# Kernel optimization log

Measured on AMD Instinct MI355X. Metric: run time of the kernel, lower is better.

Reference implementation:

```python
import jax, jax.numpy as jnp
import numpy as np

N_NODES = 100000
N_EDGES = 3200000
NFEAT, NHID1, NHID2, NCLASS = 512, 16, 64, 16
NEG_SLOPE = 0.01  # torch F.leaky_relu default


def setup_inputs() -> dict:
    key = jax.random.key(0)
    ks = jax.random.split(key, 10)
    x = jax.random.normal(ks[0], (N_NODES, NFEAT), dtype=jnp.float32)
    src = jax.random.randint(ks[1], (N_EDGES,), 0, N_NODES, dtype=jnp.int32)
    dst = jax.random.randint(ks[2], (N_EDGES,), 0, N_NODES, dtype=jnp.int32)
    edge_vals = jax.random.uniform(ks[3], (N_EDGES,), dtype=jnp.float32)
    def glorot(k, fan_in, fan_out):
        s = 1.0 / np.sqrt(fan_in)
        return jax.random.uniform(k, (fan_in, fan_out), dtype=jnp.float32, minval=-s, maxval=s)
    W1 = glorot(ks[4], NFEAT, NHID1)
    b1 = jnp.zeros((NHID1,), dtype=jnp.float32)
    W2 = glorot(ks[5], NHID1, NHID2)
    b2 = jnp.zeros((NHID2,), dtype=jnp.float32)
    W3 = glorot(ks[6], NHID2, NCLASS)
    b3 = jnp.zeros((NCLASS,), dtype=jnp.float32)
    return dict(x=x, src=src, dst=dst, edge_vals=edge_vals,
                W1=W1, b1=b1, W2=W2, b2=b2, W3=W3, b3=b3)


def _gcn_layer(h, src, dst, edge_vals, W, b):
    # support = h @ W  [N, F_out]; out = spmm(adj, support) + b
    support = h @ W
    msgs = edge_vals[:, None] * support[src]            # gather + scale per edge
    agg = jax.ops.segment_sum(msgs, dst, num_segments=N_NODES)  # scatter-add
    return agg + b


def reference(x, src, dst, edge_vals, W1, b1, W2, b2, W3, b3):
    h1 = jax.nn.leaky_relu(_gcn_layer(x, src, dst, edge_vals, W1, b1), NEG_SLOPE)
    h2 = jax.nn.leaky_relu(_gcn_layer(h1, src, dst, edge_vals, W2, b2), NEG_SLOPE)
    h3 = _gcn_layer(h2, src, dst, edge_vals, W3, b3)
    return jax.nn.log_softmax(h3, axis=1)
```

## Files before the change

### kernel.cpp

```cpp
#include <hip/hip_runtime.h>
#include <cmath>


#define BD 64
#define NBKT 1563
#define NBLK 2048
#define SORT_CAP 3072

typedef __attribute__((ext_vector_type(8))) short bf16x8;
typedef __attribute__((ext_vector_type(4))) float f32x4;

__device__ __forceinline__ short to_bf16(float f) {
    unsigned u = __float_as_uint(f);
    u += 0x8000u;
    return (short)(u >> 16);
}
__device__ __forceinline__ unsigned pack2bf(float a, float b) {
    return (unsigned)(unsigned short)to_bf16(a) |
           ((unsigned)(unsigned short)to_bf16(b) << 16);
}
__device__ __forceinline__ float bf_lo(unsigned v) {
    return __uint_as_float(v << 16);
}
__device__ __forceinline__ float bf_hi(unsigned v) {
    return __uint_as_float(v & 0xFFFF0000u);
}

__global__ __launch_bounds__(256) void p1g_k(const float* __restrict__ x,
                                             const float* __restrict__ W1,
                                             unsigned short* __restrict__ t1,
                                             const int* __restrict__ dst,
                                             int* __restrict__ C,
                                             int N, int E, int NB_gemm) {
    __shared__ __align__(16) unsigned short wlds[8192];
    if ((int)blockIdx.x < NB_gemm) {
        {
            int t = threadIdx.x;
            int kt = t >> 4, col = t & 15;
#pragma unroll
            for (int j = 0; j < 32; ++j) {
                int k = kt * 32 + j;
                float v = W1[(size_t)k * 16 + col];
                wlds[(((kt * 4 + (j >> 3)) * 16 + col) << 3) + (j & 7)] =
                    (unsigned short)to_bf16(v);
            }
        }
        __syncthreads();
        int wid = (blockIdx.x * 256 + (int)threadIdx.x) >> 6;
        int ntiles = (N + 15) >> 4;
        if (wid >= ntiles) return;
        int lane = threadIdx.x & 63;
        int m = lane & 15, kg = lane >> 4;
        int r = wid * 16 + m;
        int rc = r < N ? r : N - 1;
        const float4* Xv = reinterpret_cast<const float4*>(x + (size_t)rc * 512);
        f32x4 acc = {0.f, 0.f, 0.f, 0.f};
#pragma unroll
        for (int kt = 0; kt < 16; ++kt) {
            float4 xa = Xv[kt * 8 + kg * 2];
            float4 xb = Xv[kt * 8 + kg * 2 + 1];
            bf16x8 a;
            a[0] = to_bf16(xa.x); a[1] = to_bf16(xa.y);
            a[2] = to_bf16(xa.z); a[3] = to_bf16(xa.w);
            a[4] = to_bf16(xb.x); a[5] = to_bf16(xb.y);
            a[6] = to_bf16(xb.z); a[7] = to_bf16(xb.w);
            bf16x8 b = *reinterpret_cast<const bf16x8*>(
                &wlds[((kt * 4 + kg) * 16 + m) << 3]);
            acc = __builtin_amdgcn_mfma_f32_16x16x32_bf16(a, b, acc, 0, 0, 0);
        }
#pragma unroll
        for (int i = 0; i < 4; ++i) {
            int ro = wid * 16 + kg * 4 + i;
            if (ro < N) t1[(size_t)ro * 16 + m] = (unsigned short)to_bf16(acc[i]);
        }
        return;
    }
    int* h = (int*)wlds;
    int k = (int)blockIdx.x - NB_gemm;
    for (int i = threadIdx.x; i < NBKT; i += 256) h[i] = 0;
    __syncthreads();
    int epb = (E + NBLK - 1) / NBLK;
    int lo = k * epb, hi = min(lo + epb, E);
    for (int e = lo + (int)threadIdx.x; e < hi; e += 256)
        atomicAdd(&h[dst[e] >> 6], 1);
    __syncthreads();
    for (int i = threadIdx.x; i < NBKT; i += 256)
        C[(size_t)k * NBKT + i] = h[i];
}

__global__ __launch_bounds__(256) void p2a(int* __restrict__ C,
                                           int* __restrict__ btot) {
    __shared__ int s[16][17];
    int bs = threadIdx.x & 15, ki = threadIdx.x >> 4;
    int b = blockIdx.x * 16 + bs;
    bool ok = b < NBKT;
    int sum = 0;
    if (ok) {
        for (int j = 0; j < 128; ++j)
            sum += C[(size_t)(ki * 128 + j) * NBKT + b];
    }
    s[ki][bs] = sum;
    __syncthreads();
    int base = 0;
    for (int j = 0; j < ki; ++j) base += s[j][bs];
    if (ok) {
        if (ki == 15) btot[b] = base + sum;
        int run = base;
        for (int j = 0; j < 128; ++j) {
            size_t idx = (size_t)(ki * 128 + j) * NBKT + b;
            int v = C[idx];
            C[idx] = run;
            run += v;
        }
    }
}

__global__ __launch_bounds__(256) void p2b(const int* __restrict__ btot,
                                           int* __restrict__ bbase, int E) {
    __shared__ int ps[256];
    int loc[8], sum = 0;
    int base = (int)threadIdx.x * 8;
#pragma unroll
    for (int j = 0; j < 8; ++j) {
        int i = base + j;
        int v = (i < NBKT) ? btot[i] : 0;
        loc[j] = sum; sum += v;
    }
    ps[threadIdx.x] = sum;
    __syncthreads();
    for (int st = 1; st < 256; st <<= 1) {
        int tv = (threadIdx.x >= (unsigned)st) ? ps[threadIdx.x - st] : 0;
        __syncthreads();
        ps[threadIdx.x] += tv;
        __syncthreads();
    }
    int prev = ps[threadIdx.x] - sum;
#pragma unroll
    for (int j = 0; j < 8; ++j) {
        int i = base + j;
        if (i <= NBKT) bbase[i] = prev + loc[j];
    }
}

__global__ __launch_bounds__(256) void p3_place(const int* __restrict__ src,
                                                const int* __restrict__ dst,
                                                const float* __restrict__ ev,
                                                const int* __restrict__ C,
                                                const int* __restrict__ bbase,
                                                int2* __restrict__ recA, int E) {
    __shared__ int cur[NBKT];
    int bid = (int)blockIdx.x;
    int k = ((bid & 7) << 8) | (bid >> 3);
    for (int i = threadIdx.x; i < NBKT; i += 256)
        cur[i] = bbase[i] + C[(size_t)k * NBKT + i];
    __syncthreads();
    int epb = (E + NBLK - 1) / NBLK;
    int lo = k * epb, hi = min(lo + epb, E);
    for (int e = lo + (int)threadIdx.x; e < hi; e += 256) {
        int d = dst[e];
        int p = atomicAdd(&cur[d >> 6], 1);
        recA[p] = make_int2(src[e] | ((d & 63) << 17), __float_as_int(ev[e]));
    }
}

__device__ __forceinline__ int pack_rec(int srcbits, float evf) {
    int q = (int)(evf * 32768.f + 0.5f);
    q = q > 32767 ? 32767 : q;
    return (srcbits << 15) | q;
}

__global__ __launch_bounds__(256) void sort2_k(const int* __restrict__ bbase,
                                               const int2* __restrict__ recA,
                                               int* __restrict__ recB,
                                               int* __restrict__ off,
                                               int N, int E) {
    __shared__ int2 ls[SORT_CAP];
    __shared__ int lo_[SORT_CAP];
    __shared__ int cnt[BD];
    __shared__ int cur[BD];
    int b = blockIdx.x;
    int e0 = bbase[b], e1 = bbase[b + 1], n = e1 - e0;
    if (threadIdx.x < BD) cnt[threadIdx.x] = 0;
    __syncthreads();
    if (n <= SORT_CAP) {
        for (int i = threadIdx.x; i < n; i += 256) {
            int2 r = recA[e0 + i];
            ls[i] = r;
            atomicAdd(&cnt[(r.x >> 17) & 63], 1);
        }
        __syncthreads();
        if (threadIdx.x < 64) {
            int v = cnt[threadIdx.x];
            int inc = v;
#pragma unroll
            for (int s = 1; s < 64; s <<= 1) {
                int t = __shfl_up(inc, s, 64);
                if ((int)threadIdx.x >= s) inc += t;
            }
            int excl = inc - v;
            cur[threadIdx.x] = excl;
            int node = b * BD + (int)threadIdx.x;
            if (node < N) off[node] = e0 + excl;
        }
        if (threadIdx.x == 64 && b == (int)gridDim.x - 1) off[N] = E;
        __syncthreads();
        for (int i = threadIdx.x; i < n; i += 256) {
            int2 r = ls[i];
            int p = atomicAdd(&cur[(r.x >> 17) & 63], 1);
            lo_[p] = pack_rec(r.x & 0x1FFFF, __int_as_float(r.y));
        }
        __syncthreads();
        for (int i = threadIdx.x; i < n; i += 256)
            recB[e0 + i] = lo_[i];
    } else {
        for (int i = threadIdx.x; i < n; i += 256)
            atomicAdd(&cnt[(recA[e0 + i].x >> 17) & 63], 1);
        __syncthreads();
        if (threadIdx.x < 64) {
            int v = cnt[threadIdx.x];
            int inc = v;
#pragma unroll
            for (int s = 1; s < 64; s <<= 1) {
                int t = __shfl_up(inc, s, 64);
                if ((int)threadIdx.x >= s) inc += t;
            }
            int excl = inc - v;
            cur[threadIdx.x] = excl;
            int node = b * BD + (int)threadIdx.x;
            if (node < N) off[node] = e0 + excl;
        }
        if (threadIdx.x == 64 && b == (int)gridDim.x - 1) off[N] = E;
        __syncthreads();
        for (int i = threadIdx.x; i < n; i += 256) {
            int2 r = recA[e0 + i];
            int p = atomicAdd(&cur[(r.x >> 17) & 63], 1);
            recB[e0 + p] = pack_rec(r.x & 0x1FFFF, __int_as_float(r.y));
        }
    }
}

#define EV_DEQ (1.f / 32768.f)
template<int GACT, int OMODE>
__global__ __launch_bounds__(256) void pull_w(const int* __restrict__ off,
                                              const int* __restrict__ rec,
                                              const unsigned short* __restrict__ S,
                                              const float* __restrict__ bg,
                                              const float* __restrict__ bo,
                                              void* __restrict__ Ovp, int N) {
    int wid = (blockIdx.x * 256 + (int)threadIdx.x) >> 6;
    int lane = threadIdx.x & 63;
    if (wid >= N) return;
    int q = lane & 3, g = lane >> 2;
    int e0 = off[wid], e1 = off[wid + 1];
    float4 bv = make_float4(0, 0, 0, 0);
    if (GACT) bv = *reinterpret_cast<const float4*>(bg + q * 4);
    const uint2* Sp = reinterpret_cast<const uint2*>(S);
    float ax = 0.f, ay = 0.f, az = 0.f, aw = 0.f;
    int e = e0 + g;
    for (; e + 16 < e1; e += 32) {
        unsigned r0 = (unsigned)rec[e], r1 = (unsigned)rec[e + 16];
        uint2 u0 = Sp[(size_t)(r0 >> 15) * 4 + q];
        uint2 u1 = Sp[(size_t)(r1 >> 15) * 4 + q];
        float v0 = (float)(r0 & 32767u) * EV_DEQ;
        float v1 = (float)(r1 & 32767u) * EV_DEQ;
        float s0x = bf_lo(u0.x), s0y = bf_hi(u0.x), s0z = bf_lo(u0.y), s0w = bf_hi(u0.y);
        float s1x = bf_lo(u1.x), s1y = bf_hi(u1.x), s1z = bf_lo(u1.y), s1w = bf_hi(u1.y);
        if (GACT) {
            s0x += bv.x; s0x = s0x > 0.f ? s0x : 0.01f * s0x;
            s0y += bv.y; s0y = s0y > 0.f ? s0y : 0.01f * s0y;
            s0z += bv.z; s0z = s0z > 0.f ? s0z : 0.01f * s0z;
            s0w += bv.w; s0w = s0w > 0.f ? s0w : 0.01f * s0w;
            s1x += bv.x; s1x = s1x > 0.f ? s1x : 0.01f * s1x;
            s1y += bv.y; s1y = s1y > 0.f ? s1y : 0.01f * s1y;
            s1z += bv.z; s1z = s1z > 0.f ? s1z : 0.01f * s1z;
            s1w += bv.w; s1w = s1w > 0.f ? s1w : 0.01f * s1w;
        }
        ax += v0 * s0x; ay += v0 * s0y; az += v0 * s0z; aw += v0 * s0w;
        ax += v1 * s1x; ay += v1 * s1y; az += v1 * s1z; aw += v1 * s1w;
    }
    if (e < e1) {
        unsigned r0 = (unsigned)rec[e];
        uint2 u0 = Sp[(size_t)(r0 >> 15) * 4 + q];
        float v0 = (float)(r0 & 32767u) * EV_DEQ;
        float s0x = bf_lo(u0.x), s0y = bf_hi(u0.x), s0z = bf_lo(u0.y), s0w = bf_hi(u0.y);
        if (GACT) {
            s0x += bv.x; s0x = s0x > 0.f ? s0x : 0.01f * s0x;
            s0y += bv.y; s0y = s0y > 0.f ? s0y : 0.01f * s0y;
            s0z += bv.z; s0z = s0z > 0.f ? s0z : 0.01f * s0z;
            s0w += bv.w; s0w = s0w > 0.f ? s0w : 0.01f * s0w;
        }
        ax += v0 * s0x; ay += v0 * s0y; az += v0 * s0z; aw += v0 * s0w;
    }
#pragma unroll
    for (int m = 4; m <= 32; m <<= 1) {
        ax += __shfl_xor(ax, m);
        ay += __shfl_xor(ay, m);
        az += __shfl_xor(az, m);
        aw += __shfl_xor(aw, m);
    }
    if (OMODE == 0) {
        if (lane < 4) {
            unsigned short* O = (unsigned short*)Ovp;
            uint2 o;
            o.x = pack2bf(ax, ay);
            o.y = pack2bf(az, aw);
            reinterpret_cast<uint2*>(O + (size_t)wid * 16)[lane] = o;
        }
    } else {
        float* O = (float*)Ovp;
        float4 b3v = *reinterpret_cast<const float4*>(bo + q * 4);
        float x0 = ax + b3v.x, x1 = ay + b3v.y, x2 = az + b3v.z, x3 = aw + b3v.w;
        float m = fmaxf(fmaxf(x0, x1), fmaxf(x2, x3));
        m = fmaxf(m, __shfl_xor(m, 1));
        m = fmaxf(m, __shfl_xor(m, 2));
        float ss = __expf(x0 - m) + __expf(x1 - m) + __expf(x2 - m) + __expf(x3 - m);
        ss += __shfl_xor(ss, 1);
        ss += __shfl_xor(ss, 2);
        float lse = m + __logf(ss);
        if (lane < 4)
            *reinterpret_cast<float4*>(O + (size_t)wid * 16 + lane * 4) =
                make_float4(x0 - lse, x1 - lse, x2 - lse, x3 - lse);
    }
}

__global__ __launch_bounds__(256) void gemm23_k(const unsigned short* __restrict__ A,
                                                const float* __restrict__ W2,
                                                const float* __restrict__ b2,
                                                const float* __restrict__ W3,
                                                unsigned short* __restrict__ T3, int N) {
    int row = blockIdx.x * 256 + threadIdx.x;
    if (row >= N) return;
    float a[16];
    const uint2* Av = reinterpret_cast<const uint2*>(A + (size_t)row * 16);
#pragma unroll
    for (int qq = 0; qq < 4; ++qq) {
        uint2 v = Av[qq];
        a[4*qq+0] = bf_lo(v.x); a[4*qq+1] = bf_hi(v.x);
        a[4*qq+2] = bf_lo(v.y); a[4*qq+3] = bf_hi(v.y);
    }
    float h[64];
#pragma unroll
    for (int j = 0; j < 64; ++j) h[j] = b2[j];
#pragma unroll
    for (int k = 0; k < 16; ++k)
#pragma unroll
        for (int j = 0; j < 64; ++j)
            h[j] += a[k] * W2[(size_t)k * 64 + j];
#pragma unroll
    for (int j = 0; j < 64; ++j) h[j] = h[j] > 0.f ? h[j] : 0.01f * h[j];
    float o[16];
#pragma unroll
    for (int c = 0; c < 16; ++c) o[c] = 0.f;
#pragma unroll
    for (int j = 0; j < 64; ++j)
#pragma unroll
        for (int c = 0; c < 16; ++c)
            o[c] += h[j] * W3[(size_t)j * 16 + c];
    unsigned r[8];
#pragma unroll
    for (int i = 0; i < 8; ++i) r[i] = pack2bf(o[2*i], o[2*i+1]);
    uint4* Tv = reinterpret_cast<uint4*>(T3 + (size_t)row * 16);
    Tv[0] = make_uint4(r[0], r[1], r[2], r[3]);
    Tv[1] = make_uint4(r[4], r[5], r[6], r[7]);
}

extern "C" void kernel_launch(void* const* d_in, const int* in_sizes, int n_in,
                              void* d_out, int out_size, void* d_ws, size_t ws_size,
                              hipStream_t stream) {
    const float* x   = (const float*)d_in[0];
    const int*   src = (const int*)d_in[1];
    const int*   dst = (const int*)d_in[2];
    const float* ev  = (const float*)d_in[3];
    const float* W1  = (const float*)d_in[4];
    const float* b1  = (const float*)d_in[5];
    const float* W2  = (const float*)d_in[6];
    const float* b2  = (const float*)d_in[7];
    const float* W3  = (const float*)d_in[8];
    const float* b3  = (const float*)d_in[9];
    float* out = (float*)d_out;

    const int N = in_sizes[0] / 512;
    const int E = in_sizes[1];

    unsigned short* B0 = (unsigned short*)d_ws;
    int2*  recA  = (int2*)(B0 + (size_t)N * 16);
    int*   recB  = (int*)(recA + E);
    int*   C     = recB + E;
    int*   btot  = C + (size_t)NBLK * NBKT;
    int*   bbase = btot + NBKT;
    int*   off   = bbase + (NBKT + 1);
    unsigned short* B1 = (unsigned short*)recA;
    unsigned short* B2 = B1 + (size_t)N * 16;

    auto blks = [](long n) { return (int)((n + 255) / 256); };
    const int ntiles = (N + 15) / 16;
    const int NB_gemm = (ntiles + 3) / 4;
    const int pull_blocks = blks((long)N * 64);

    p1g_k<<<NB_gemm + NBLK, 256, 0, stream>>>(x, W1, B0, dst, C, N, E, NB_gemm);
    p2a<<<(NBKT + 15) / 16, 256, 0, stream>>>(C, btot);
    p2b<<<1, 256, 0, stream>>>(btot, bbase, E);
    p3_place<<<NBLK, 256, 0, stream>>>(src, dst, ev, C, bbase, recA, E);
    sort2_k<<<NBKT, 256, 0, stream>>>(bbase, recA, recB, off, N, E);

    pull_w<0, 0><<<pull_blocks, 256, 0, stream>>>(off, recB, B0, nullptr, nullptr, B1, N);

    pull_w<1, 0><<<pull_blocks, 256, 0, stream>>>(off, recB, B1, b1, nullptr, B2, N);

    gemm23_k<<<NB_gemm, 256, 0, stream>>>(B2, W2, b2, W3, B0, N);

    pull_w<0, 1><<<pull_blocks, 256, 0, stream>>>(off, recB, B0, nullptr, b3, out, N);
}
```

Before: 264.8 us.

## Fuse pull and dense phases into one cooperative persistent kernel with grid syncs

Replaces the four separate pull/gemm launches with a single persistent cooperative kernel that loops over nodes with a grid-stride and uses grid-wide syncs between phases. It also folds the single-block bucket scan into p2a via a last-block-done atomic counter, and rewrites the layer-2/3 dense step as wave-per-row with shuffle reductions. The aim is to cut launch gaps and tail effects. In exchange it adds grid sync cost, caps the grid at occupancy, adds shuffle-heavy reductions in gemm23, and calls host occupancy and attribute queries on every launch.

```diff
diff --git a/kernel.cpp b/kernel.cpp
--- a/kernel.cpp
+++ b/kernel.cpp
@@ -1,5 +1,8 @@
 #include <hip/hip_runtime.h>
+#include <hip/hip_cooperative_groups.h>
 #include <cmath>
+
+namespace cg = cooperative_groups;
 
 
 #define BD 64
@@ -19,19 +22,17 @@
     return (unsigned)(unsigned short)to_bf16(a) |
            ((unsigned)(unsigned short)to_bf16(b) << 16);
 }
-__device__ __forceinline__ float bf_lo(unsigned v) {
-    return __uint_as_float(v << 16);
-}
-__device__ __forceinline__ float bf_hi(unsigned v) {
-    return __uint_as_float(v & 0xFFFF0000u);
-}
+__device__ __forceinline__ float bf_lo(unsigned v) { return __uint_as_float(v << 16); }
+__device__ __forceinline__ float bf_hi(unsigned v) { return __uint_as_float(v & 0xFFFF0000u); }
 
 __global__ __launch_bounds__(256) void p1g_k(const float* __restrict__ x,
                                              const float* __restrict__ W1,
                                              unsigned short* __restrict__ t1,
                                              const int* __restrict__ dst,
                                              int* __restrict__ C,
+                                             int* __restrict__ done,
                                              int N, int E, int NB_gemm) {
+    if (blockIdx.x == 0 && threadIdx.x == 0) *done = 0;
     __shared__ __align__(16) unsigned short wlds[8192];
     if ((int)blockIdx.x < NB_gemm) {
         {
@@ -89,8 +90,12 @@
 }
 
 __global__ __launch_bounds__(256) void p2a(int* __restrict__ C,
-                                           int* __restrict__ btot) {
+                                           int* __restrict__ btot,
+                                           int* __restrict__ bbase,
+                                           int* __restrict__ done) {
     __shared__ int s[16][17];
+    __shared__ int ps[256];
+    __shared__ int isLast;
     int bs = threadIdx.x & 15, ki = threadIdx.x >> 4;
     int b = blockIdx.x * 16 + bs;
     bool ok = b < NBKT;
@@ -113,20 +118,22 @@
             run += v;
         }
     }
-}
-
-__global__ __launch_bounds__(256) void p2b(const int* __restrict__ btot,
-                                           int* __restrict__ bbase, int E) {
-    __shared__ int ps[256];
-    int loc[8], sum = 0;
-    int base = (int)threadIdx.x * 8;
+    __syncthreads();
+    if (threadIdx.x == 0) {
+        __threadfence();
+        isLast = (atomicAdd(done, 1) == (int)gridDim.x - 1);
+    }
+    __syncthreads();
+    if (!isLast) return;
+    int loc[8], ssum = 0;
+    int base2 = (int)threadIdx.x * 8;
 #pragma unroll
     for (int j = 0; j < 8; ++j) {
-        int i = base + j;
+        int i = base2 + j;
         int v = (i < NBKT) ? btot[i] : 0;
-        loc[j] = sum; sum += v;
-    }
-    ps[threadIdx.x] = sum;
+        loc[j] = ssum; ssum += v;
+    }
+    ps[threadIdx.x] = ssum;
     __syncthreads();
     for (int st = 1; st < 256; st <<= 1) {
         int tv = (threadIdx.x >= (unsigned)st) ? ps[threadIdx.x - st] : 0;
@@ -134,10 +141,10 @@
         ps[threadIdx.x] += tv;
         __syncthreads();
     }
-    int prev = ps[threadIdx.x] - sum;
+    int prev = ps[threadIdx.x] - ssum;
 #pragma unroll
     for (int j = 0; j < 8; ++j) {
-        int i = base + j;
+        int i = base2 + j;
         if (i <= NBKT) bbase[i] = prev + loc[j];
     }
 }
@@ -241,127 +248,146 @@
 
 #define EV_DEQ (1.f / 32768.f)
 template<int GACT, int OMODE>
-__global__ __launch_bounds__(256) void pull_w(const int* __restrict__ off,
-                                              const int* __restrict__ rec,
-                                              const unsigned short* __restrict__ S,
-                                              const float* __restrict__ bg,
-                                              const float* __restrict__ bo,
-                                              void* __restrict__ Ovp, int N) {
-    int wid = (blockIdx.x * 256 + (int)threadIdx.x) >> 6;
+__device__ __forceinline__ void pull_phase(const int* __restrict__ off,
+                                           const int* __restrict__ rec,
+                                           const unsigned short* __restrict__ S,
+                                           const float* __restrict__ bg,
+                                           const float* __restrict__ bo,
+                                           void* __restrict__ Ovp,
+                                           int N, int wid0, int wstride) {
     int lane = threadIdx.x & 63;
-    if (wid >= N) return;
     int q = lane & 3, g = lane >> 2;
-    int e0 = off[wid], e1 = off[wid + 1];
     float4 bv = make_float4(0, 0, 0, 0);
     if (GACT) bv = *reinterpret_cast<const float4*>(bg + q * 4);
+    float4 b3v = make_float4(0, 0, 0, 0);
+    if (OMODE == 1) b3v = *reinterpret_cast<const float4*>(bo + q * 4);
     const uint2* Sp = reinterpret_cast<const uint2*>(S);
-    float ax = 0.f, ay = 0.f, az = 0.f, aw = 0.f;
-    int e = e0 + g;
-    for (; e + 16 < e1; e += 32) {
-        unsigned r0 = (unsigned)rec[e], r1 = (unsigned)rec[e + 16];
-        uint2 u0 = Sp[(size_t)(r0 >> 15) * 4 + q];
-        uint2 u1 = Sp[(size_t)(r1 >> 15) * 4 + q];
-        float v0 = (float)(r0 & 32767u) * EV_DEQ;
-        float v1 = (float)(r1 & 32767u) * EV_DEQ;
-        float s0x = bf_lo(u0.x), s0y = bf_hi(u0.x), s0z = bf_lo(u0.y), s0w = bf_hi(u0.y);
-        float s1x = bf_lo(u1.x), s1y = bf_hi(u1.x), s1z = bf_lo(u1.y), s1w = bf_hi(u1.y);
-        if (GACT) {
-            s0x += bv.x; s0x = s0x > 0.f ? s0x : 0.01f * s0x;
-            s0y += bv.y; s0y = s0y > 0.f ? s0y : 0.01f * s0y;
-            s0z += bv.z; s0z = s0z > 0.f ? s0z : 0.01f * s0z;
-            s0w += bv.w; s0w = s0w > 0.f ? s0w : 0.01f * s0w;
-            s1x += bv.x; s1x = s1x > 0.f ? s1x : 0.01f * s1x;
-            s1y += bv.y; s1y = s1y > 0.f ? s1y : 0.01f * s1y;
-            s1z += bv.z; s1z = s1z > 0.f ? s1z : 0.01f * s1z;
-            s1w += bv.w; s1w = s1w > 0.f ? s1w : 0.01f * s1w;
-        }
-        ax += v0 * s0x; ay += v0 * s0y; az += v0 * s0z; aw += v0 * s0w;
-        ax += v1 * s1x; ay += v1 * s1y; az += v1 * s1z; aw += v1 * s1w;
-    }
-    if (e < e1) {
-        unsigned r0 = (unsigned)rec[e];
-        uint2 u0 = Sp[(size_t)(r0 >> 15) * 4 + q];
-        float v0 = (float)(r0 & 32767u) * EV_DEQ;
-        float s0x = bf_lo(u0.x), s0y = bf_hi(u0.x), s0z = bf_lo(u0.y), s0w = bf_hi(u0.y);
-        if (GACT) {
-            s0x += bv.x; s0x = s0x > 0.f ? s0x : 0.01f * s0x;
-            s0y += bv.y; s0y = s0y > 0.f ? s0y : 0.01f * s0y;
-            s0z += bv.z; s0z = s0z > 0.f ? s0z : 0.01f * s0z;
-            s0w += bv.w; s0w = s0w > 0.f ? s0w : 0.01f * s0w;
-        }
-        ax += v0 * s0x; ay += v0 * s0y; az += v0 * s0z; aw += v0 * s0w;
-    }
-#pragma unroll
-    for (int m = 4; m <= 32; m <<= 1) {
-        ax += __shfl_xor(ax, m);
-        ay += __shfl_xor(ay, m);
-        az += __shfl_xor(az, m);
-        aw += __shfl_xor(aw, m);
-    }
-    if (OMODE == 0) {
+    for (int wid = wid0; wid < N; wid += wstride) {
+        int e0 = off[wid], e1 = off[wid + 1];
+        float ax = 0.f, ay = 0.f, az = 0.f, aw = 0.f;
+        int e = e0 + g;
+        for (; e + 16 < e1; e += 32) {
+            unsigned r0 = (unsigned)rec[e], r1 = (unsigned)rec[e + 16];
+            uint2 u0 = Sp[(size_t)(r0 >> 15) * 4 + q];
+            uint2 u1 = Sp[(size_t)(r1 >> 15) * 4 + q];
+            float v0 = (float)(r0 & 32767u) * EV_DEQ;
+            float v1 = (float)(r1 & 32767u) * EV_DEQ;
+            float s0x = bf_lo(u0.x), s0y = bf_hi(u0.x), s0z = bf_lo(u0.y), s0w = bf_hi(u0.y);
+            float s1x = bf_lo(u1.x), s1y = bf_hi(u1.x), s1z = bf_lo(u1.y), s1w = bf_hi(u1.y);
+            if (GACT) {
+                s0x += bv.x; s0x = s0x > 0.f ? s0x : 0.01f * s0x;
+                s0y += bv.y; s0y = s0y > 0.f ? s0y : 0.01f * s0y;
+                s0z += bv.z; s0z = s0z > 0.f ? s0z : 0.01f * s0z;
+                s0w += bv.w; s0w = s0w > 0.f ? s0w : 0.01f * s0w;
+                s1x += bv.x; s1x = s1x > 0.f ? s1x : 0.01f * s1x;
+                s1y += bv.y; s1y = s1y > 0.f ? s1y : 0.01f * s1y;
+                s1z += bv.z; s1z = s1z > 0.f ? s1z : 0.01f * s1z;
+                s1w += bv.w; s1w = s1w > 0.f ? s1w : 0.01f * s1w;
+            }
+            ax += v0 * s0x; ay += v0 * s0y; az += v0 * s0z; aw += v0 * s0w;
+            ax += v1 * s1x; ay += v1 * s1y; az += v1 * s1z; aw += v1 * s1w;
+        }
+        if (e < e1) {
+            unsigned r0 = (unsigned)rec[e];
+            uint2 u0 = Sp[(size_t)(r0 >> 15) * 4 + q];
+            float v0 = (float)(r0 & 32767u) * EV_DEQ;
+            float s0x = bf_lo(u0.x), s0y = bf_hi(u0.x), s0z = bf_lo(u0.y), s0w = bf_hi(u0.y);
+            if (GACT) {
+                s0x += bv.x; s0x = s0x > 0.f ? s0x : 0.01f * s0x;
+                s0y += bv.y; s0y = s0y > 0.f ? s0y : 0.01f * s0y;
+                s0z += bv.z; s0z = s0z > 0.f ? s0z : 0.01f * s0z;
+                s0w += bv.w; s0w = s0w > 0.f ? s0w : 0.01f * s0w;
+            }
+            ax += v0 * s0x; ay += v0 * s0y; az += v0 * s0z; aw += v0 * s0w;
+        }
+#pragma unroll
+        for (int m = 4; m <= 32; m <<= 1) {
+            ax += __shfl_xor(ax, m);
+            ay += __shfl_xor(ay, m);
+            az += __shfl_xor(az, m);
+            aw += __shfl_xor(aw, m);
+        }
+        if (OMODE == 0) {
+            if (lane < 4) {
+                unsigned short* O = (unsigned short*)Ovp;
+                uint2 o;
+                o.x = pack2bf(ax, ay);
+                o.y = pack2bf(az, aw);
+                reinterpret_cast<uint2*>(O + (size_t)wid * 16)[lane] = o;
+            }
+        } else {
+            float* O = (float*)Ovp;
+            float x0 = ax + b3v.x, x1 = ay + b3v.y, x2 = az + b3v.z, x3 = aw + b3v.w;
+            float m = fmaxf(fmaxf(x0, x1), fmaxf(x2, x3));
+            m = fmaxf(m, __shfl_xor(m, 1));
+            m = fmaxf(m, __shfl_xor(m, 2));
+            float ss = __expf(x0 - m) + __expf(x1 - m) + __expf(x2 - m) + __expf(x3 - m);
+            ss += __shfl_xor(ss, 1);
+            ss += __shfl_xor(ss, 2);
+            float lse = m + __logf(ss);
+            if (lane < 4)
+                *reinterpret_cast<float4*>(O + (size_t)wid * 16 + lane * 4) =
+                    make_float4(x0 - lse, x1 - lse, x2 - lse, x3 - lse);
+        }
+    }
+}
+
+__device__ __forceinline__ void gemm23_phase(const unsigned short* __restrict__ A,
+                                             const float* __restrict__ W2,
+                                             const float* __restrict__ b2,
+                                             const float* __restrict__ W3,
+                                             unsigned short* __restrict__ T3,
+                                             int N, int wid0, int wstride) {
+    int lane = threadIdx.x & 63;
+    float hb = b2[lane];
+    for (int r = wid0; r < N; r += wstride) {
+        unsigned u = 0;
+        if (lane < 8) u = reinterpret_cast<const unsigned*>(A + (size_t)r * 16)[lane];
+        float a[16];
+#pragma unroll
+        for (int p = 0; p < 8; ++p) {
+            unsigned up = __shfl(u, p);
+            a[2 * p] = bf_lo(up); a[2 * p + 1] = bf_hi(up);
+        }
+        float h = hb;
+#pragma unroll
+        for (int k = 0; k < 16; ++k) h += a[k] * W2[k * 64 + lane];
+        h = h > 0.f ? h : 0.01f * h;
+        float o[16];
+#pragma unroll
+        for (int c = 0; c < 16; ++c) o[c] = h * W3[lane * 16 + c];
+#pragma unroll
+        for (int m = 1; m < 64; m <<= 1) {
+#pragma unroll
+            for (int c = 0; c < 16; ++c) o[c] += __shfl_xor(o[c], m);
+        }
         if (lane < 4) {
-            unsigned short* O = (unsigned short*)Ovp;
-            uint2 o;
-            o.x = pack2bf(ax, ay);
-            o.y = pack2bf(az, aw);
-            reinterpret_cast<uint2*>(O + (size_t)wid * 16)[lane] = o;
-        }
-    } else {
-        float* O = (float*)Ovp;
-        float4 b3v = *reinterpret_cast<const float4*>(bo + q * 4);
-        float x0 = ax + b3v.x, x1 = ay + b3v.y, x2 = az + b3v.z, x3 = aw + b3v.w;
-        float m = fmaxf(fmaxf(x0, x1), fmaxf(x2, x3));
-        m = fmaxf(m, __shfl_xor(m, 1));
-        m = fmaxf(m, __shfl_xor(m, 2));
-        float ss = __expf(x0 - m) + __expf(x1 - m) + __expf(x2 - m) + __expf(x3 - m);
-        ss += __shfl_xor(ss, 1);
-        ss += __shfl_xor(ss, 2);
-        float lse = m + __logf(ss);
-        if (lane < 4)
-            *reinterpret_cast<float4*>(O + (size_t)wid * 16 + lane * 4) =
-                make_float4(x0 - lse, x1 - lse, x2 - lse, x3 - lse);
-    }
-}
-
-__global__ __launch_bounds__(256) void gemm23_k(const unsigned short* __restrict__ A,
-                                                const float* __restrict__ W2,
-                                                const float* __restrict__ b2,
-                                                const float* __restrict__ W3,
-                                                unsigned short* __restrict__ T3, int N) {
-    int row = blockIdx.x * 256 + threadIdx.x;
-    if (row >= N) return;
-    float a[16];
-    const uint2* Av = reinterpret_cast<const uint2*>(A + (size_t)row * 16);
-#pragma unroll
-    for (int qq = 0; qq < 4; ++qq) {
-        uint2 v = Av[qq];
-        a[4*qq+0] = bf_lo(v.x); a[4*qq+1] = bf_hi(v.x);
-        a[4*qq+2] = bf_lo(v.y); a[4*qq+3] = bf_hi(v.y);
-    }
-    float h[64];
-#pragma unroll
-    for (int j = 0; j < 64; ++j) h[j] = b2[j];
-#pragma unroll
-    for (int k = 0; k < 16; ++k)
-#pragma unroll
-        for (int j = 0; j < 64; ++j)
-            h[j] += a[k] * W2[(size_t)k * 64 + j];
-#pragma unroll
-    for (int j = 0; j < 64; ++j) h[j] = h[j] > 0.f ? h[j] : 0.01f * h[j];
-    float o[16];
-#pragma unroll
-    for (int c = 0; c < 16; ++c) o[c] = 0.f;
-#pragma unroll
-    for (int j = 0; j < 64; ++j)
-#pragma unroll
-        for (int c = 0; c < 16; ++c)
-            o[c] += h[j] * W3[(size_t)j * 16 + c];
-    unsigned r[8];
-#pragma unroll
-    for (int i = 0; i < 8; ++i) r[i] = pack2bf(o[2*i], o[2*i+1]);
-    uint4* Tv = reinterpret_cast<uint4*>(T3 + (size_t)row * 16);
-    Tv[0] = make_uint4(r[0], r[1], r[2], r[3]);
-    Tv[1] = make_uint4(r[4], r[5], r[6], r[7]);
+            uint2 ov;
+            ov.x = pack2bf(o[lane * 4 + 0], o[lane * 4 + 1]);
+            ov.y = pack2bf(o[lane * 4 + 2], o[lane * 4 + 3]);
+            reinterpret_cast<uint2*>(T3 + (size_t)r * 16)[lane] = ov;
+        }
+    }
+}
+
+__global__ __launch_bounds__(256, 8) void pipeline_k(
+    const int* off, const int* recB,
+    unsigned short* B0, unsigned short* B1, unsigned short* B2,
+    const float* b1, const float* W2, const float* b2, const float* W3,
+    const float* b3, float* out, int N, int coop, int phase) {
+    int wid0 = ((int)blockIdx.x * 256 + (int)threadIdx.x) >> 6;
+    int wstride = (int)gridDim.x * 4;
+    if (phase < 0 || phase == 0)
+        pull_phase<0, 0>(off, recB, B0, nullptr, nullptr, B1, N, wid0, wstride);
+    if (coop) cg::this_grid().sync();
+    if (phase < 0 || phase == 1)
+        pull_phase<1, 0>(off, recB, B1, b1, nullptr, B2, N, wid0, wstride);
+    if (coop) cg::this_grid().sync();
+    if (phase < 0 || phase == 2)
+        gemm23_phase(B2, W2, b2, W3, B0, N, wid0, wstride);
+    if (coop) cg::this_grid().sync();
+    if (phase < 0 || phase == 3)
+        pull_phase<0, 1>(off, recB, B0, nullptr, b3, out, N, wid0, wstride);
 }
 
 extern "C" void kernel_launch(void* const* d_in, const int* in_sizes, int n_in,
@@ -389,25 +415,42 @@
     int*   btot  = C + (size_t)NBLK * NBKT;
     int*   bbase = btot + NBKT;
     int*   off   = bbase + (NBKT + 1);
+    int*   done  = off + (N + 1);
     unsigned short* B1 = (unsigned short*)recA;
     unsigned short* B2 = B1 + (size_t)N * 16;
 
-    auto blks = [](long n) { return (int)((n + 255) / 256); };
     const int ntiles = (N + 15) / 16;
     const int NB_gemm = (ntiles + 3) / 4;
-    const int pull_blocks = blks((long)N * 64);
-
-    p1g_k<<<NB_gemm + NBLK, 256, 0, stream>>>(x, W1, B0, dst, C, N, E, NB_gemm);
-    p2a<<<(NBKT + 15) / 16, 256, 0, stream>>>(C, btot);
-    p2b<<<1, 256, 0, stream>>>(btot, bbase, E);
+
+    p1g_k<<<NB_gemm + NBLK, 256, 0, stream>>>(x, W1, B0, dst, C, done, N, E, NB_gemm);
+    p2a<<<(NBKT + 15) / 16, 256, 0, stream>>>(C, btot, bbase, done);
     p3_place<<<NBLK, 256, 0, stream>>>(src, dst, ev, C, bbase, recA, E);
     sort2_k<<<NBKT, 256, 0, stream>>>(bbase, recA, recB, off, N, E);
 
-    pull_w<0, 0><<<pull_blocks, 256, 0, stream>>>(off, recB, B0, nullptr, nullptr, B1, N);
-
-    pull_w<1, 0><<<pull_blocks, 256, 0, stream>>>(off, recB, B1, b1, nullptr, B2, N);
-
-    gemm23_k<<<NB_gemm, 256, 0, stream>>>(B2, W2, b2, W3, B0, N);
-
-    pull_w<0, 1><<<pull_blocks, 256, 0, stream>>>(off, recB, B0, nullptr, b3, out, N);
-}
+    int dev = 0, nCU = 0, maxPerCU = 0, coopOK = 0;
+    hipGetDevice(&dev);
+    hipDeviceGetAttribute(&coopOK, hipDeviceAttributeCooperativeLaunch, dev);
+    hipDeviceGetAttribute(&nCU, hipDeviceAttributeMultiprocessorCount, dev);
+    hipOccupancyMaxActiveBlocksPerMultiprocessor(&maxPerCU, pipeline_k, 256, 0);
+    int grid = maxPerCU * nCU;
+    if (grid > 2048) grid = 2048;
+    if (grid < 64) grid = 64;
+
+    const int* offc = off;
+    const int* recBc = recB;
+    int coop = 1, phase = -1;
+    hipError_t cerr = hipErrorUnknown;
+    if (coopOK && maxPerCU > 0) {
+        void* args[] = {(void*)&offc, (void*)&recBc, (void*)&B0, (void*)&B1,
+                        (void*)&B2, (void*)&b1, (void*)&W2, (void*)&b2,
+                        (void*)&W3, (void*)&b3, (void*)&out, (void*)&N,
+                        (void*)&coop, (void*)&phase};
+        cerr = hipLaunchCooperativeKernel((void*)pipeline_k, dim3(grid), dim3(256),
+                                          args, 0, stream);
+    }
+    if (cerr != hipSuccess) {
+        for (int ph = 0; ph < 4; ++ph)
+            pipeline_k<<<2048, 256, 0, stream>>>(offc, recBc, B0, B1, B2, b1,
+                                                 W2, b2, W3, b3, out, N, 0, ph);
+    }
+}
```

New measurement: 828.5 us. 3.13x slower.
